# Kernel tuning notes

Measured on AMD Instinct MI355X. Metric: run time of the kernel, lower is better.

Reference implementation:

```python
import jax, jax.numpy as jnp
import numpy as np

N, L, HH, WW, E, NH = 8, 300, 96, 96, 256, 8


def setup_inputs() -> dict:
    key = jax.random.key(0)
    ks = jax.random.split(key, 9)
    return {
        "query_row": jax.random.normal(ks[0], (N, L, E), dtype=jnp.float32),
        "query_col": jax.random.normal(ks[1], (N, L, E), dtype=jnp.float32),
        "key_row": jax.random.normal(ks[2], (N, HH, WW, E), dtype=jnp.float32),
        "key_col": jax.random.normal(ks[3], (N, HH, WW, E), dtype=jnp.float32),
        "value": jax.random.normal(ks[4], (N, HH, WW, E), dtype=jnp.float32),
        "in_proj_weight": jax.random.normal(ks[5], (5 * E, E), dtype=jnp.float32) * 0.02,
        "in_proj_bias": jax.random.normal(ks[6], (5 * E,), dtype=jnp.float32) * 0.02,
        "out_proj_weight": jax.random.normal(ks[7], (E, E), dtype=jnp.float32) * 0.02,
        "out_proj_bias": jax.random.normal(ks[8], (E,), dtype=jnp.float32) * 0.02,
        "num_heads": NH,
    }


def reference(query_row, query_col, key_row, key_col, value,
              in_proj_weight, in_proj_bias, out_proj_weight, out_proj_bias,
              num_heads):
    bsz, tgt_len, embed_dim = query_row.shape
    head_dim = embed_dim // num_heads
    scaling = float(head_dim) ** -0.5

    def proj(x, i):
        w = in_proj_weight[i * embed_dim:(i + 1) * embed_dim]
        b = in_proj_bias[i * embed_dim:(i + 1) * embed_dim]
        return x @ w.T + b

    q_row = proj(query_row, 0) * scaling          # (N, L, E)
    q_col = proj(query_col, 1) * scaling          # (N, L, E)
    k_row = proj(key_row, 2).mean(axis=1)         # mean over H -> (N, W, E)
    k_col = proj(key_col, 3).mean(axis=2)         # mean over W -> (N, H, E)
    v = proj(value, 4)                            # (N, H, W, E)

    heads = lambda t: t.reshape(*t.shape[:-1], num_heads, head_dim)
    qr, qc, kr, kc = heads(q_row), heads(q_col), heads(k_row), heads(k_col)
    vh = heads(v)                                 # (N, H, W, nh, hd)

    # additive row/col decomposed scores -> independent softmaxes
    w_row = jax.nn.softmax(jnp.einsum('blnd,bwnd->bnlw', qr, kr), axis=-1)  # (N,nh,L,W)
    w_col = jax.nn.softmax(jnp.einsum('blnd,bhnd->bnlh', qc, kc), axis=-1)  # (N,nh,L,H)

    # contract col weights with value over H, then row weights over W
    tmp = jnp.einsum('bnlh,bhwnd->bnlwd', w_col, vh)       # (N,nh,L,W,hd)
    out = jnp.einsum('bnlw,bnlwd->blnd', w_row, tmp)       # (N,L,nh,hd)
    out = out.reshape(bsz, tgt_len, embed_dim).transpose(1, 0, 2)  # (L,N,E)
    return out @ out_proj_weight.T + out_proj_bias
```

## Files before the change

kernel.cpp:

```cpp
#include <hip/hip_runtime.h>
#include <cstdint>


typedef __attribute__((ext_vector_type(8))) short short8v;
typedef __attribute__((ext_vector_type(4))) short short4v;
typedef __attribute__((ext_vector_type(4))) float f32x4;

#define SCALE_Q 0.17677669529663687f

#define GLL16(gp, lp)                                                   \
  __builtin_amdgcn_global_load_lds(                                     \
      (const __attribute__((address_space(1))) void*)(gp),              \
      (__attribute__((address_space(3))) void*)(lp), 16, 0, 0)

__device__ __forceinline__ unsigned short f2bf(float x) {
  unsigned int u = __builtin_bit_cast(unsigned int, x);
  u += 0x7FFFu + ((u >> 16) & 1u);
  return (unsigned short)(u >> 16);
}

__device__ __forceinline__ unsigned int cvtpk(float a, float b) {
  unsigned int r;
  asm("v_cvt_pk_bf16_f32 %0, %1, %2" : "=v"(r) : "v"(a), "v"(b));
  return r;
}

__device__ __forceinline__ short8v pack8cvt(const f32x4& lo, const f32x4& hi) {
  union { short8v s; unsigned int u[4]; } z;
  z.u[0] = cvtpk(lo[0], lo[1]);
  z.u[1] = cvtpk(lo[2], lo[3]);
  z.u[2] = cvtpk(hi[0], hi[1]);
  z.u[3] = cvtpk(hi[2], hi[3]);
  return z.s;
}

__device__ __forceinline__ short4v pack4cvt(float a, float b, float c, float d) {
  union { short4v s; unsigned int u[2]; } z;
  z.u[0] = cvtpk(a, b);
  z.u[1] = cvtpk(c, d);
  return z.s;
}

__device__ __forceinline__ short8v pack8(const float4& fa, const float4& fb) {
  short8v v;
  v[0] = (short)f2bf(fa.x); v[1] = (short)f2bf(fa.y);
  v[2] = (short)f2bf(fa.z); v[3] = (short)f2bf(fa.w);
  v[4] = (short)f2bf(fb.x); v[5] = (short)f2bf(fb.y);
  v[6] = (short)f2bf(fb.z); v[7] = (short)f2bf(fb.w);
  return v;
}

__global__ __launch_bounds__(256) void cvt_w_kernel(const float* __restrict__ w_in,
                                                    const float* __restrict__ w_out,
                                                    short* __restrict__ Wb) {
  int idx = blockIdx.x * 256 + threadIdx.x;
  float v = (idx < 327680) ? w_in[idx] : w_out[idx - 327680];
  Wb[idx] = (short)f2bf(v);
}

__global__ __launch_bounds__(256) void mean_over_h_v3(const float* __restrict__ in,
                                                      float* __restrict__ out) {
  __shared__ float4 part[256];
  int bw = blockIdx.x;
  int b = bw / 96, w = bw - b * 96;
  int t = threadIdx.x, e4 = t & 63, hq = t >> 6;
  const float4* p = (const float4*)(in + ((size_t)b * 9216 + w) * 256) + e4 +
                    (size_t)hq * 24 * 6144;
  float4 s = {0.f, 0.f, 0.f, 0.f};
#pragma unroll
  for (int i = 0; i < 24; ++i) {
    float4 v = p[(size_t)i * 6144];
    s.x += v.x; s.y += v.y; s.z += v.z; s.w += v.w;
  }
  part[t] = s;
  __syncthreads();
  if (t < 64) {
    float4 a = part[t], c = part[t + 64], d = part[t + 128], e = part[t + 192];
    float4 o;
    o.x = (a.x + c.x + d.x + e.x) * (1.f / 96.f);
    o.y = (a.y + c.y + d.y + e.y) * (1.f / 96.f);
    o.z = (a.z + c.z + d.z + e.z) * (1.f / 96.f);
    o.w = (a.w + c.w + d.w + e.w) * (1.f / 96.f);
    ((float4*)out)[(size_t)bw * 64 + t] = o;
  }
}

__global__ __launch_bounds__(256) void mean_over_w_v3(const float* __restrict__ in,
                                                      float* __restrict__ out) {
  __shared__ float4 part[256];
  int bh = blockIdx.x;
  int t = threadIdx.x, e4 = t & 63, wq = t >> 6;
  const float4* p = (const float4*)(in + (size_t)bh * 24576) + e4 + (size_t)wq * 24 * 64;
  float4 s = {0.f, 0.f, 0.f, 0.f};
#pragma unroll
  for (int i = 0; i < 24; ++i) {
    float4 v = p[(size_t)i * 64];
    s.x += v.x; s.y += v.y; s.z += v.z; s.w += v.w;
  }
  part[t] = s;
  __syncthreads();
  if (t < 64) {
    float4 a = part[t], c = part[t + 64], d = part[t + 128], e = part[t + 192];
    float4 o;
    o.x = (a.x + c.x + d.x + e.x) * (1.f / 96.f);
    o.y = (a.y + c.y + d.y + e.y) * (1.f / 96.f);
    o.z = (a.z + c.z + d.z + e.z) * (1.f / 96.f);
    o.w = (a.w + c.w + d.w + e.w) * (1.f / 96.f);
    ((float4*)out)[(size_t)bh * 64 + t] = o;
  }
}

__global__ __launch_bounds__(256) void gemm_proj(
    const float* __restrict__ A0, const float* __restrict__ A1,
    const float* __restrict__ Aadd,
    const short* __restrict__ Wb, const float* __restrict__ bias,
    float* __restrict__ Cf, short* __restrict__ Cb0, short* __restrict__ Cb1,
    float scale, int mode) {
  __shared__ short As[32 * 264];
  int y = blockIdx.y;
  const float* A = y ? A1 : A0;
  short* Cb = y ? Cb1 : Cb0;
  const short* Wp = Wb + y * 65536;
  const float* bp = bias + y * 256;
  int t = threadIdx.x;
  int m0 = blockIdx.x * 32;
  int wave = t >> 6, lane = t & 63, r = lane & 15, g = lane >> 4;

  {
    int row = t >> 3, c0 = (t & 7) * 32;
    size_t off = ((size_t)m0 + row) * 256 + c0;
    const float* ap = A + off;
    float4 ld[8];
#pragma unroll
    for (int j = 0; j < 8; ++j) ld[j] = *(const float4*)(ap + j * 4);
    if (Aadd) {
      const float* aq = Aadd + off;
#pragma unroll
      for (int j = 0; j < 8; ++j) {
        float4 e = *(const float4*)(aq + j * 4);
        ld[j].x += e.x; ld[j].y += e.y; ld[j].z += e.z; ld[j].w += e.w;
      }
    }
    short* dst = &As[row * 264 + c0];
#pragma unroll
    for (int j = 0; j < 4; ++j)
      *(short8v*)(dst + j * 8) = pack8(ld[2 * j], ld[2 * j + 1]);
  }
  __syncthreads();

  f32x4 acc[2][4] = {};
  const short* wbase = Wp + (size_t)(wave * 64 + r) * 256;
#pragma unroll
  for (int ks = 0; ks < 8; ++ks) {
    short8v af0 = *(const short8v*)&As[r * 264 + ks * 32 + g * 8];
    short8v af1 = *(const short8v*)&As[(16 + r) * 264 + ks * 32 + g * 8];
    short8v bf[4];
#pragma unroll
    for (int nf = 0; nf < 4; ++nf)
      bf[nf] = *(const short8v*)(wbase + nf * 16 * 256 + ks * 32 + g * 8);
#pragma unroll
    for (int nf = 0; nf < 4; ++nf) {
      acc[0][nf] = __builtin_amdgcn_mfma_f32_16x16x32_bf16(af0, bf[nf], acc[0][nf], 0, 0, 0);
      acc[1][nf] = __builtin_amdgcn_mfma_f32_16x16x32_bf16(af1, bf[nf], acc[1][nf], 0, 0, 0);
    }
  }

#pragma unroll
  for (int mf = 0; mf < 2; ++mf)
#pragma unroll
    for (int nf = 0; nf < 4; ++nf) {
      int nn = wave * 64 + nf * 16 + r;
      float bval = bp[nn];
#pragma unroll
      for (int i = 0; i < 4; ++i) {
        int m = m0 + mf * 16 + g * 4 + i;
        float val = (acc[mf][nf][i] + bval) * scale;
        if (mode == 1) {
          int bb = m / 300, ll = m - bb * 300;
          Cf[((size_t)ll * 8 + bb) * 256 + nn] = val;
        } else {
          Cb[(size_t)m * 256 + nn] = (short)f2bf(val);
        }
      }
    }
}

__global__ __launch_bounds__(512, 4) void vproj_kernel(
    const float* __restrict__ A, const short* __restrict__ Wb,
    const float* __restrict__ bias, short* __restrict__ vvT) {
  __shared__ float buf[2][16 * 260];
  __shared__ short Ts[8][32 * 36];
  int t = threadIdx.x;
  int wave = t >> 6, lane = t & 63, r = lane & 15, g = lane >> 4;
  int m0g = blockIdx.x * 96;
  int b_ = blockIdx.x / 96;
  int hw00 = (blockIdx.x - b_ * 96) * 96;
  int chbase = wave * 32;

  short8v bf[8][2];
  {
    const short* wbase = Wb + (size_t)(chbase + r) * 256;
#pragma unroll
    for (int ks = 0; ks < 8; ++ks)
#pragma unroll
      for (int nf = 0; nf < 2; ++nf)
        bf[ks][nf] = *(const short8v*)(wbase + nf * 16 * 256 + ks * 32 + g * 8);
  }
#pragma unroll
  for (int ks = 0; ks < 8; ++ks)
#pragma unroll
    for (int nf = 0; nf < 2; ++nf)
      asm volatile("" : "+a"(bf[ks][nf]));
  float bias_v[2];
#pragma unroll
  for (int nf = 0; nf < 2; ++nf) bias_v[nf] = bias[chbase + nf * 16 + r];

#pragma unroll
  for (int q = 0; q < 2; ++q) {
#pragma unroll
    for (int i = 0; i < 2; ++i) {
      int row = wave * 2 + i;
      const float* gp = A + ((size_t)m0g + q * 16 + row) * 256 + lane * 4;
      GLL16(gp, &buf[q][row * 260]);
    }
  }

  int chg = chbase + (lane & 31);
  int half = lane >> 5;
  short* vbase = vvT + (size_t)(b_ * 8 + (chg >> 5)) * 294912 +
                 (size_t)(chg & 31) * 9216 + hw00;
  const short* tsr = &Ts[wave][(lane & 31) * 36];

#pragma unroll
  for (int tt = 0; tt < 6; ++tt) {
    if (tt == 5)                  asm volatile("s_waitcnt vmcnt(0)" ::: "memory");
    else if (tt == 2 || tt == 4)  asm volatile("s_waitcnt vmcnt(4)" ::: "memory");
    else                          asm volatile("s_waitcnt vmcnt(2)" ::: "memory");
    __builtin_amdgcn_s_barrier();

    f32x4 acc[2] = {};
    const float* bp_ = &buf[tt & 1][0];
#pragma unroll
    for (int ks = 0; ks < 8; ++ks) {
      const float* p = bp_ + r * 260 + ks * 32 + g * 8;
      f32x4 lo = *(const f32x4*)p;
      f32x4 hi = *(const f32x4*)(p + 4);
      short8v af = pack8cvt(lo, hi);
      acc[0] = __builtin_amdgcn_mfma_f32_16x16x32_bf16(af, bf[ks][0], acc[0], 0, 0, 0);
      acc[1] = __builtin_amdgcn_mfma_f32_16x16x32_bf16(af, bf[ks][1], acc[1], 0, 0, 0);
    }

#pragma unroll
    for (int nf = 0; nf < 2; ++nf) {
      float bv = bias_v[nf];
      *(short4v*)&Ts[wave][(nf * 16 + r) * 36 + (tt & 1) * 16 + g * 4] =
          pack4cvt(acc[nf][0] + bv, acc[nf][1] + bv, acc[nf][2] + bv, acc[nf][3] + bv);
    }
    asm volatile("" ::: "memory");

    if (tt & 1) {
      short* gdst = vbase + (tt - 1) * 16 + half * 16;
      const short* src = tsr + half * 16;
      *(short8v*)gdst = *(const short8v*)src;
      *(short8v*)(gdst + 8) = *(const short8v*)(src + 8);
      asm volatile("" ::: "memory");
    }

    __builtin_amdgcn_s_barrier();
    if (tt + 2 < 6) {
#pragma unroll
      for (int i = 0; i < 2; ++i) {
        int row = wave * 2 + i;
        const float* gp = A + ((size_t)m0g + (tt + 2) * 16 + row) * 256 + lane * 4;
        GLL16(gp, &buf[tt & 1][row * 260]);
      }
    }
  }
}

__global__ __launch_bounds__(64) void scores_softmax_v2(
    const short* __restrict__ qrb, const short* __restrict__ qcb,
    const short* __restrict__ krb, const short* __restrict__ kcb,
    short* __restrict__ wrowB, float* __restrict__ wcolT) {
  int lchunk = blockIdx.x, bn = blockIdx.y, kind = blockIdx.z;
  int b = bn >> 3, n = bn & 7;
  int lane = threadIdx.x;
  int r = lane & 15, g = lane >> 4;
  const short* qb = kind ? qcb : qrb;
  const short* kb = kind ? kcb : krb;
  int l0 = lchunk * 80;

  short8v a[5], bfr[6];
#pragma unroll
  for (int lf = 0; lf < 5; ++lf) {
    int l = l0 + lf * 16 + r;
    if (l > 299) l = 299;
    a[lf] = *(const short8v*)(qb + ((size_t)b * 300 + l) * 256 + n * 32 + g * 8);
  }
#pragma unroll
  for (int f = 0; f < 6; ++f)
    bfr[f] = *(const short8v*)(kb + ((size_t)b * 96 + f * 16 + r) * 256 + n * 32 + g * 8);

  f32x4 c[5][6];
#pragma unroll
  for (int lf = 0; lf < 5; ++lf)
#pragma unroll
    for (int f = 0; f < 6; ++f) {
      f32x4 z = {};
      c[lf][f] = __builtin_amdgcn_mfma_f32_16x16x32_bf16(a[lf], bfr[f], z, 0, 0, 0);
    }

#pragma unroll
  for (int lf = 0; lf < 5; ++lf)
#pragma unroll
    for (int i = 0; i < 4; ++i) {
      float m = c[lf][0][i];
#pragma unroll
      for (int f = 1; f < 6; ++f) m = fmaxf(m, c[lf][f][i]);
#pragma unroll
      for (int mask = 1; mask <= 8; mask <<= 1) m = fmaxf(m, __shfl_xor(m, mask, 64));
      float e[6], s = 0.f;
#pragma unroll
      for (int f = 0; f < 6; ++f) { e[f] = __expf(c[lf][f][i] - m); s += e[f]; }
#pragma unroll
      for (int mask = 1; mask <= 8; mask <<= 1) s += __shfl_xor(s, mask, 64);
      float inv = 1.f / s;
#pragma unroll
      for (int f = 0; f < 6; ++f) c[lf][f][i] = e[f] * inv;
    }

  if (kind == 0) {
#pragma unroll
    for (int lf = 0; lf < 5; ++lf)
#pragma unroll
      for (int i = 0; i < 4; ++i) {
        int l = l0 + lf * 16 + g * 4 + i;
        bool ok = (l < 300);
#pragma unroll
        for (int f = 0; f < 6; ++f) {
          float wv = ok ? c[lf][f][i] : 0.f;
          wrowB[((size_t)bn * 320 + l) * 96 + f * 16 + r] = (short)f2bf(wv);
        }
      }
  } else {
#pragma unroll
    for (int lf = 0; lf < 5; ++lf)
#pragma unroll
      for (int f = 0; f < 6; ++f) {
        int l = l0 + lf * 16 + g * 4;
        f32x4 wv = c[lf][f];
#pragma unroll
        for (int i = 0; i < 4; ++i) if (l + i >= 300) wv[i] = 0.f;
        *(f32x4*)(wcolT + ((size_t)bn * 96 + f * 16 + r) * 320 + l) = wv;
      }
  }
}

__global__ __launch_bounds__(512, 2) void attn_kernel(
    const short* __restrict__ wrowB, const float* __restrict__ wcolT,
    const short* __restrict__ vvT, float* __restrict__ part0,
    float* __restrict__ part1) {
  __shared__ f32x4 cmb[3][2][4][64];
  int i = blockIdx.x;
  int xcd = i & 7, j = i >> 3;
  int grp = j / 10, rem = j - grp * 10;
  int bn = grp * 8 + xcd;
  int lh = rem >> 1, hh2 = rem & 1;
  int b = bn >> 3, n = bn & 7;
  int t = threadIdx.x, wave = t >> 6, lane = t & 63;
  int df = wave & 1, hq = wave >> 1;
  int lbase = lh * 64;
  int r = lane & 15, g = lane >> 4;
  int hbase = hh2 * 48 + hq * 12;

  short8v a[4][3];
  const short* wr = wrowB + (size_t)bn * 320 * 96;
#pragma unroll
  for (int lf = 0; lf < 4; ++lf)
#pragma unroll
    for (int ks = 0; ks < 3; ++ks)
      a[lf][ks] = *(const short8v*)(wr + (lbase + lf * 16 + r) * 96 + ks * 32 + g * 8);

  const short* vb = vvT + (size_t)bn * 294912 + (size_t)(df * 16 + r) * 9216 + hbase * 96;
  const float* wcb = wcolT + ((size_t)bn * 96 + hbase) * 320 + lbase + g * 4;

  f32x4 acc[4] = {};
  short8v b0[3], b1[3];
  f32x4 w0[4], w1[4];
#pragma unroll
  for (int ks = 0; ks < 3; ++ks) b0[ks] = *(const short8v*)(vb + ks * 32 + g * 8);
#pragma unroll
  for (int lf = 0; lf < 4; ++lf) w0[lf] = *(const f32x4*)(wcb + lf * 16);

#pragma unroll
  for (int h2 = 0; h2 < 6; ++h2) {
    int h = h2 * 2;
#pragma unroll
    for (int ks = 0; ks < 3; ++ks) b1[ks] = *(const short8v*)(vb + (h + 1) * 96 + ks * 32 + g * 8);
#pragma unroll
    for (int lf = 0; lf < 4; ++lf) w1[lf] = *(const f32x4*)(wcb + (h + 1) * 320 + lf * 16);
    {
      f32x4 R[4] = {};
#pragma unroll
      for (int ks = 0; ks < 3; ++ks)
#pragma unroll
        for (int lf = 0; lf < 4; ++lf)
          R[lf] = __builtin_amdgcn_mfma_f32_16x16x32_bf16(a[lf][ks], b0[ks], R[lf], 0, 0, 0);
#pragma unroll
      for (int lf = 0; lf < 4; ++lf) acc[lf] += w0[lf] * R[lf];
    }
    if (h2 < 5) {
#pragma unroll
      for (int ks = 0; ks < 3; ++ks) b0[ks] = *(const short8v*)(vb + (h + 2) * 96 + ks * 32 + g * 8);
#pragma unroll
      for (int lf = 0; lf < 4; ++lf) w0[lf] = *(const f32x4*)(wcb + (h + 2) * 320 + lf * 16);
    }
    {
      f32x4 R[4] = {};
#pragma unroll
      for (int ks = 0; ks < 3; ++ks)
#pragma unroll
        for (int lf = 0; lf < 4; ++lf)
          R[lf] = __builtin_amdgcn_mfma_f32_16x16x32_bf16(a[lf][ks], b1[ks], R[lf], 0, 0, 0);
#pragma unroll
      for (int lf = 0; lf < 4; ++lf) acc[lf] += w1[lf] * R[lf];
    }
  }

  if (hq > 0) {
#pragma unroll
    for (int lf = 0; lf < 4; ++lf) cmb[hq - 1][df][lf][lane] = acc[lf];
  }
  __syncthreads();
  if (hq == 0) {
    float* po = hh2 ? part1 : part0;
#pragma unroll
    for (int lf = 0; lf < 4; ++lf) {
      f32x4 o = acc[lf];
#pragma unroll
      for (int q = 0; q < 3; ++q) o += cmb[q][df][lf][lane];
#pragma unroll
      for (int i2 = 0; i2 < 4; ++i2) {
        int l = lbase + lf * 16 + g * 4 + i2;
        if (l < 300)
          po[((size_t)b * 300 + l) * 256 + n * 32 + df * 16 + r] = o[i2];
      }
    }
  }
}

extern "C" void kernel_launch(void* const* d_in, const int* in_sizes, int n_in,
                              void* d_out, int out_size, void* d_ws, size_t ws_size,
                              hipStream_t stream) {
  const float* query_row = (const float*)d_in[0];
  const float* query_col = (const float*)d_in[1];
  const float* key_row   = (const float*)d_in[2];
  const float* key_col   = (const float*)d_in[3];
  const float* value     = (const float*)d_in[4];
  const float* W         = (const float*)d_in[5];
  const float* Bv        = (const float*)d_in[6];
  const float* Wout      = (const float*)d_in[7];
  const float* Bout      = (const float*)d_in[8];

  float* ws = (float*)d_ws;
  float* krm   = ws;
  float* kcm   = krm + 196608;
  float* part0 = kcm + 196608;
  float* part1 = part0 + 614400;
  float* wcolT = part1 + 614400;
  short* qrb   = (short*)(wcolT + 1966080);
  short* qcb   = qrb + 614400;
  short* krb   = qcb + 614400;
  short* kcb   = krb + 196608;
  short* wrowB = kcb + 196608;
  short* vvT   = wrowB + 1966080;
  short* Wb    = vvT + 18874368;

  cvt_w_kernel<<<1536, 256, 0, stream>>>(W, Wout, Wb);
  mean_over_h_v3<<<768, 256, 0, stream>>>(key_row, krm);
  mean_over_w_v3<<<768, 256, 0, stream>>>(key_col, kcm);
  gemm_proj<<<dim3(75, 2), 256, 0, stream>>>(query_row, query_col, nullptr, Wb, Bv,
                                             nullptr, qrb, qcb, SCALE_Q, 3);
  gemm_proj<<<dim3(24, 2), 256, 0, stream>>>(krm, kcm, nullptr, Wb + 131072, Bv + 512,
                                             nullptr, krb, kcb, 1.f, 3);
  vproj_kernel<<<768, 512, 0, stream>>>(value, Wb + 262144, Bv + 1024, vvT);
  scores_softmax_v2<<<dim3(4, 64, 2), 64, 0, stream>>>(qrb, qcb, krb, kcb, wrowB, wcolT);
  attn_kernel<<<640, 512, 0, stream>>>(wrowB, wcolT, vvT, part0, part1);
  gemm_proj<<<dim3(75, 1), 256, 0, stream>>>(part0, nullptr, part1, Wb + 327680, Bout,
                                             (float*)d_out, nullptr, nullptr, 1.f, 1);
}
```

Measured before the change: 157.7 us.

## Merge value projection with key means and batch the small projection GEMMs

The value projection and the two key mean reductions now run in one kernel: even blocks do the V projection and odd blocks do the row or column means, which cuts two launches and lets the memory-bound reductions overlap with the MFMA work. The four query and key projection GEMMs are merged into one 512-thread launch that dispatches on block index, and the output projection uses a 512-thread variant with bounds clamping. The goal is fewer kernel launches and less idle tail time. In exchange, the interleaved blocks use different shared-memory and register amounts, which may hurt occupancy of the heavy V path.

```diff
diff --git a/kernel.cpp b/kernel.cpp
--- a/kernel.cpp
+++ b/kernel.cpp
@@ -58,90 +58,184 @@
   Wb[idx] = (short)f2bf(v);
 }
 
-__global__ __launch_bounds__(256) void mean_over_h_v3(const float* __restrict__ in,
-                                                      float* __restrict__ out) {
-  __shared__ float4 part[256];
-  int bw = blockIdx.x;
-  int b = bw / 96, w = bw - b * 96;
-  int t = threadIdx.x, e4 = t & 63, hq = t >> 6;
-  const float4* p = (const float4*)(in + ((size_t)b * 9216 + w) * 256) + e4 +
-                    (size_t)hq * 24 * 6144;
-  float4 s = {0.f, 0.f, 0.f, 0.f};
-#pragma unroll
-  for (int i = 0; i < 24; ++i) {
-    float4 v = p[(size_t)i * 6144];
-    s.x += v.x; s.y += v.y; s.z += v.z; s.w += v.w;
-  }
-  part[t] = s;
-  __syncthreads();
-  if (t < 64) {
-    float4 a = part[t], c = part[t + 64], d = part[t + 128], e = part[t + 192];
-    float4 o;
-    o.x = (a.x + c.x + d.x + e.x) * (1.f / 96.f);
-    o.y = (a.y + c.y + d.y + e.y) * (1.f / 96.f);
-    o.z = (a.z + c.z + d.z + e.z) * (1.f / 96.f);
-    o.w = (a.w + c.w + d.w + e.w) * (1.f / 96.f);
-    ((float4*)out)[(size_t)bw * 64 + t] = o;
-  }
-}
-
-__global__ __launch_bounds__(256) void mean_over_w_v3(const float* __restrict__ in,
-                                                      float* __restrict__ out) {
-  __shared__ float4 part[256];
-  int bh = blockIdx.x;
-  int t = threadIdx.x, e4 = t & 63, wq = t >> 6;
-  const float4* p = (const float4*)(in + (size_t)bh * 24576) + e4 + (size_t)wq * 24 * 64;
-  float4 s = {0.f, 0.f, 0.f, 0.f};
-#pragma unroll
-  for (int i = 0; i < 24; ++i) {
-    float4 v = p[(size_t)i * 64];
-    s.x += v.x; s.y += v.y; s.z += v.z; s.w += v.w;
-  }
-  part[t] = s;
-  __syncthreads();
-  if (t < 64) {
-    float4 a = part[t], c = part[t + 64], d = part[t + 128], e = part[t + 192];
-    float4 o;
-    o.x = (a.x + c.x + d.x + e.x) * (1.f / 96.f);
-    o.y = (a.y + c.y + d.y + e.y) * (1.f / 96.f);
-    o.z = (a.z + c.z + d.z + e.z) * (1.f / 96.f);
-    o.w = (a.w + c.w + d.w + e.w) * (1.f / 96.f);
-    ((float4*)out)[(size_t)bh * 64 + t] = o;
-  }
-}
-
-__global__ __launch_bounds__(256) void gemm_proj(
-    const float* __restrict__ A0, const float* __restrict__ A1,
-    const float* __restrict__ Aadd,
-    const short* __restrict__ Wb, const float* __restrict__ bias,
-    float* __restrict__ Cf, short* __restrict__ Cb0, short* __restrict__ Cb1,
-    float scale, int mode) {
-  __shared__ short As[32 * 264];
-  int y = blockIdx.y;
-  const float* A = y ? A1 : A0;
-  short* Cb = y ? Cb1 : Cb0;
-  const short* Wp = Wb + y * 65536;
-  const float* bp = bias + y * 256;
+__global__ __launch_bounds__(512, 4) void mega1_kernel(
+    const float* __restrict__ A, const short* __restrict__ Wb,
+    const float* __restrict__ bias, short* __restrict__ vvT,
+    const float* __restrict__ key_row, const float* __restrict__ key_col,
+    float* __restrict__ krm, float* __restrict__ kcm) {
+  __shared__ float buf[2][16 * 260];
+  __shared__ short Ts[8][32 * 36];
+  int blk = blockIdx.x;
   int t = threadIdx.x;
-  int m0 = blockIdx.x * 32;
-  int wave = t >> 6, lane = t & 63, r = lane & 15, g = lane >> 4;
+
+  if ((blk & 1) == 0) {
+    int vb_id = blk >> 1;
+    int wave = t >> 6, lane = t & 63, r = lane & 15, g = lane >> 4;
+    int m0g = vb_id * 96;
+    int b_ = vb_id / 96;
+    int hw00 = (vb_id - b_ * 96) * 96;
+    int chbase = wave * 32;
+
+    short8v bf[8][2];
+    {
+      const short* wbase = Wb + (size_t)(chbase + r) * 256;
+#pragma unroll
+      for (int ks = 0; ks < 8; ++ks)
+#pragma unroll
+        for (int nf = 0; nf < 2; ++nf)
+          bf[ks][nf] = *(const short8v*)(wbase + nf * 16 * 256 + ks * 32 + g * 8);
+    }
+#pragma unroll
+    for (int ks = 0; ks < 8; ++ks)
+#pragma unroll
+      for (int nf = 0; nf < 2; ++nf)
+        asm volatile("" : "+a"(bf[ks][nf]));
+    float bias_v[2];
+#pragma unroll
+    for (int nf = 0; nf < 2; ++nf) bias_v[nf] = bias[chbase + nf * 16 + r];
+
+#pragma unroll
+    for (int q = 0; q < 2; ++q) {
+#pragma unroll
+      for (int i = 0; i < 2; ++i) {
+        int row = wave * 2 + i;
+        const float* gp = A + ((size_t)m0g + q * 16 + row) * 256 + lane * 4;
+        GLL16(gp, &buf[q][row * 260]);
+      }
+    }
+
+    int chg = chbase + (lane & 31);
+    int half = lane >> 5;
+    short* vbase = vvT + (size_t)(b_ * 8 + (chg >> 5)) * 294912 +
+                   (size_t)(chg & 31) * 9216 + hw00;
+    const short* tsr = &Ts[wave][(lane & 31) * 36];
+
+#pragma unroll
+    for (int tt = 0; tt < 6; ++tt) {
+      if (tt == 5)                  asm volatile("s_waitcnt vmcnt(0)" ::: "memory");
+      else if (tt == 2 || tt == 4)  asm volatile("s_waitcnt vmcnt(4)" ::: "memory");
+      else                          asm volatile("s_waitcnt vmcnt(2)" ::: "memory");
+      __builtin_amdgcn_s_barrier();
+
+      f32x4 acc[2] = {};
+      const float* bp_ = &buf[tt & 1][0];
+#pragma unroll
+      for (int ks = 0; ks < 8; ++ks) {
+        const float* p = bp_ + r * 260 + ks * 32 + g * 8;
+        f32x4 lo = *(const f32x4*)p;
+        f32x4 hi = *(const f32x4*)(p + 4);
+        short8v af = pack8cvt(lo, hi);
+        acc[0] = __builtin_amdgcn_mfma_f32_16x16x32_bf16(af, bf[ks][0], acc[0], 0, 0, 0);
+        acc[1] = __builtin_amdgcn_mfma_f32_16x16x32_bf16(af, bf[ks][1], acc[1], 0, 0, 0);
+      }
+
+#pragma unroll
+      for (int nf = 0; nf < 2; ++nf) {
+        float bv = bias_v[nf];
+        *(short4v*)&Ts[wave][(nf * 16 + r) * 36 + (tt & 1) * 16 + g * 4] =
+            pack4cvt(acc[nf][0] + bv, acc[nf][1] + bv, acc[nf][2] + bv, acc[nf][3] + bv);
+      }
+      asm volatile("" ::: "memory");
+
+      if (tt & 1) {
+        short* gdst = vbase + (tt - 1) * 16 + half * 16;
+        const short* src = tsr + half * 16;
+        *(short8v*)gdst = *(const short8v*)src;
+        *(short8v*)(gdst + 8) = *(const short8v*)(src + 8);
+        asm volatile("" ::: "memory");
+      }
+
+      __builtin_amdgcn_s_barrier();
+      if (tt + 2 < 6) {
+#pragma unroll
+        for (int i = 0; i < 2; ++i) {
+          int row = wave * 2 + i;
+          const float* gp = A + ((size_t)m0g + (tt + 2) * 16 + row) * 256 + lane * 4;
+          GLL16(gp, &buf[tt & 1][row * 260]);
+        }
+      }
+    }
+  } else {
+    int id = blk >> 1;
+    int sub = t >> 8, u = t & 255;
+    int e4 = u & 63, q4 = u >> 6;
+    float4* part4 = (float4*)&buf[0][0];
+    if (id < 384) {
+      int bw = id * 2 + sub;
+      int b = bw / 96, w = bw - b * 96;
+      const float4* p = (const float4*)(key_row + ((size_t)b * 9216 + w) * 256) +
+                        e4 + (size_t)q4 * 24 * 6144;
+      float4 s = {0.f, 0.f, 0.f, 0.f};
+#pragma unroll
+      for (int i = 0; i < 24; ++i) {
+        float4 v = p[(size_t)i * 6144];
+        s.x += v.x; s.y += v.y; s.z += v.z; s.w += v.w;
+      }
+      part4[sub * 256 + u] = s;
+      __syncthreads();
+      if (u < 64) {
+        float4 a = part4[sub * 256 + u], c = part4[sub * 256 + u + 64];
+        float4 d = part4[sub * 256 + u + 128], e = part4[sub * 256 + u + 192];
+        float4 o;
+        o.x = (a.x + c.x + d.x + e.x) * (1.f / 96.f);
+        o.y = (a.y + c.y + d.y + e.y) * (1.f / 96.f);
+        o.z = (a.z + c.z + d.z + e.z) * (1.f / 96.f);
+        o.w = (a.w + c.w + d.w + e.w) * (1.f / 96.f);
+        ((float4*)krm)[(size_t)bw * 64 + u] = o;
+      }
+    } else {
+      int bh = (id - 384) * 2 + sub;
+      const float4* p = (const float4*)(key_col + (size_t)bh * 24576) + e4 +
+                        (size_t)q4 * 24 * 64;
+      float4 s = {0.f, 0.f, 0.f, 0.f};
+#pragma unroll
+      for (int i = 0; i < 24; ++i) {
+        float4 v = p[(size_t)i * 64];
+        s.x += v.x; s.y += v.y; s.z += v.z; s.w += v.w;
+      }
+      part4[sub * 256 + u] = s;
+      __syncthreads();
+      if (u < 64) {
+        float4 a = part4[sub * 256 + u], c = part4[sub * 256 + u + 64];
+        float4 d = part4[sub * 256 + u + 128], e = part4[sub * 256 + u + 192];
+        float4 o;
+        o.x = (a.x + c.x + d.x + e.x) * (1.f / 96.f);
+        o.y = (a.y + c.y + d.y + e.y) * (1.f / 96.f);
+        o.z = (a.z + c.z + d.z + e.z) * (1.f / 96.f);
+        o.w = (a.w + c.w + d.w + e.w) * (1.f / 96.f);
+        ((float4*)kcm)[(size_t)bh * 64 + u] = o;
+      }
+    }
+  }
+}
+
+__global__ __launch_bounds__(512) void gemm512(
+    const float* __restrict__ krm, const float* __restrict__ kcm,
+    const float* __restrict__ qrow, const float* __restrict__ qcol,
+    const short* __restrict__ Wb, const float* __restrict__ Bv,
+    short* __restrict__ krb, short* __restrict__ kcb,
+    short* __restrict__ qrb, short* __restrict__ qcb) {
+  __shared__ short As[2][32 * 264];
+  int id = blockIdx.x;
+  const float* A; short* Cb; const short* Wp; const float* bp; int M, m064;
+  float scale;
+  if (id < 12)      { A = krm;  Cb = krb; Wp = Wb + 131072; bp = Bv + 512; M = 768;  m064 = id * 64;        scale = 1.f; }
+  else if (id < 24) { A = kcm;  Cb = kcb; Wp = Wb + 196608; bp = Bv + 768; M = 768;  m064 = (id - 12) * 64; scale = 1.f; }
+  else if (id < 62) { A = qrow; Cb = qrb; Wp = Wb;          bp = Bv;       M = 2400; m064 = (id - 24) * 64; scale = SCALE_Q; }
+  else              { A = qcol; Cb = qcb; Wp = Wb + 65536;  bp = Bv + 256; M = 2400; m064 = (id - 62) * 64; scale = SCALE_Q; }
+
+  int t = threadIdx.x, sub = t >> 8, u = t & 255;
+  int wave = u >> 6, lane = u & 63, r = lane & 15, g = lane >> 4;
+  int m0 = m064 + sub * 32;
 
   {
-    int row = t >> 3, c0 = (t & 7) * 32;
-    size_t off = ((size_t)m0 + row) * 256 + c0;
-    const float* ap = A + off;
+    int row = u >> 3, c0 = (u & 7) * 32;
+    int mrow = m0 + row; if (mrow >= M) mrow = M - 1;
+    const float* ap = A + (size_t)mrow * 256 + c0;
     float4 ld[8];
 #pragma unroll
     for (int j = 0; j < 8; ++j) ld[j] = *(const float4*)(ap + j * 4);
-    if (Aadd) {
-      const float* aq = Aadd + off;
-#pragma unroll
-      for (int j = 0; j < 8; ++j) {
-        float4 e = *(const float4*)(aq + j * 4);
-        ld[j].x += e.x; ld[j].y += e.y; ld[j].z += e.z; ld[j].w += e.w;
-      }
-    }
-    short* dst = &As[row * 264 + c0];
+    short* dst = &As[sub][row * 264 + c0];
 #pragma unroll
     for (int j = 0; j < 4; ++j)
       *(short8v*)(dst + j * 8) = pack8(ld[2 * j], ld[2 * j + 1]);
@@ -152,8 +246,8 @@
   const short* wbase = Wp + (size_t)(wave * 64 + r) * 256;
 #pragma unroll
   for (int ks = 0; ks < 8; ++ks) {
-    short8v af0 = *(const short8v*)&As[r * 264 + ks * 32 + g * 8];
-    short8v af1 = *(const short8v*)&As[(16 + r) * 264 + ks * 32 + g * 8];
+    short8v af0 = *(const short8v*)&As[sub][r * 264 + ks * 32 + g * 8];
+    short8v af1 = *(const short8v*)&As[sub][(16 + r) * 264 + ks * 32 + g * 8];
     short8v bf[4];
 #pragma unroll
     for (int nf = 0; nf < 4; ++nf)
@@ -174,108 +268,74 @@
 #pragma unroll
       for (int i = 0; i < 4; ++i) {
         int m = m0 + mf * 16 + g * 4 + i;
-        float val = (acc[mf][nf][i] + bval) * scale;
-        if (mode == 1) {
-          int bb = m / 300, ll = m - bb * 300;
-          Cf[((size_t)ll * 8 + bb) * 256 + nn] = val;
-        } else {
-          Cb[(size_t)m * 256 + nn] = (short)f2bf(val);
-        }
-      }
-    }
-}
-
-__global__ __launch_bounds__(512, 4) void vproj_kernel(
-    const float* __restrict__ A, const short* __restrict__ Wb,
-    const float* __restrict__ bias, short* __restrict__ vvT) {
-  __shared__ float buf[2][16 * 260];
-  __shared__ short Ts[8][32 * 36];
-  int t = threadIdx.x;
-  int wave = t >> 6, lane = t & 63, r = lane & 15, g = lane >> 4;
-  int m0g = blockIdx.x * 96;
-  int b_ = blockIdx.x / 96;
-  int hw00 = (blockIdx.x - b_ * 96) * 96;
-  int chbase = wave * 32;
-
-  short8v bf[8][2];
+        if (m >= M) continue;
+        Cb[(size_t)m * 256 + nn] = (short)f2bf((acc[mf][nf][i] + bval) * scale);
+      }
+    }
+}
+
+__global__ __launch_bounds__(512) void gemm512_out(
+    const float* __restrict__ A0, const float* __restrict__ Aadd,
+    const short* __restrict__ Wp, const float* __restrict__ bp,
+    float* __restrict__ Cf) {
+  __shared__ short As[2][32 * 264];
+  const int M = 2400;
+  int t = threadIdx.x, sub = t >> 8, u = t & 255;
+  int wave = u >> 6, lane = u & 63, r = lane & 15, g = lane >> 4;
+  int m0 = blockIdx.x * 64 + sub * 32;
+
   {
-    const short* wbase = Wb + (size_t)(chbase + r) * 256;
-#pragma unroll
-    for (int ks = 0; ks < 8; ++ks)
-#pragma unroll
-      for (int nf = 0; nf < 2; ++nf)
-        bf[ks][nf] = *(const short8v*)(wbase + nf * 16 * 256 + ks * 32 + g * 8);
-  }
-#pragma unroll
-  for (int ks = 0; ks < 8; ++ks)
-#pragma unroll
-    for (int nf = 0; nf < 2; ++nf)
-      asm volatile("" : "+a"(bf[ks][nf]));
-  float bias_v[2];
-#pragma unroll
-  for (int nf = 0; nf < 2; ++nf) bias_v[nf] = bias[chbase + nf * 16 + r];
-
-#pragma unroll
-  for (int q = 0; q < 2; ++q) {
-#pragma unroll
-    for (int i = 0; i < 2; ++i) {
-      int row = wave * 2 + i;
-      const float* gp = A + ((size_t)m0g + q * 16 + row) * 256 + lane * 4;
-      GLL16(gp, &buf[q][row * 260]);
-    }
-  }
-
-  int chg = chbase + (lane & 31);
-  int half = lane >> 5;
-  short* vbase = vvT + (size_t)(b_ * 8 + (chg >> 5)) * 294912 +
-                 (size_t)(chg & 31) * 9216 + hw00;
-  const short* tsr = &Ts[wave][(lane & 31) * 36];
-
-#pragma unroll
-  for (int tt = 0; tt < 6; ++tt) {
-    if (tt == 5)                  asm volatile("s_waitcnt vmcnt(0)" ::: "memory");
-    else if (tt == 2 || tt == 4)  asm volatile("s_waitcnt vmcnt(4)" ::: "memory");
-    else                          asm volatile("s_waitcnt vmcnt(2)" ::: "memory");
-    __builtin_amdgcn_s_barrier();
-
-    f32x4 acc[2] = {};
-    const float* bp_ = &buf[tt & 1][0];
-#pragma unroll
-    for (int ks = 0; ks < 8; ++ks) {
-      const float* p = bp_ + r * 260 + ks * 32 + g * 8;
-      f32x4 lo = *(const f32x4*)p;
-      f32x4 hi = *(const f32x4*)(p + 4);
-      short8v af = pack8cvt(lo, hi);
-      acc[0] = __builtin_amdgcn_mfma_f32_16x16x32_bf16(af, bf[ks][0], acc[0], 0, 0, 0);
-      acc[1] = __builtin_amdgcn_mfma_f32_16x16x32_bf16(af, bf[ks][1], acc[1], 0, 0, 0);
-    }
-
-#pragma unroll
-    for (int nf = 0; nf < 2; ++nf) {
-      float bv = bias_v[nf];
-      *(short4v*)&Ts[wave][(nf * 16 + r) * 36 + (tt & 1) * 16 + g * 4] =
-          pack4cvt(acc[nf][0] + bv, acc[nf][1] + bv, acc[nf][2] + bv, acc[nf][3] + bv);
-    }
-    asm volatile("" ::: "memory");
-
-    if (tt & 1) {
-      short* gdst = vbase + (tt - 1) * 16 + half * 16;
-      const short* src = tsr + half * 16;
-      *(short8v*)gdst = *(const short8v*)src;
-      *(short8v*)(gdst + 8) = *(const short8v*)(src + 8);
-      asm volatile("" ::: "memory");
-    }
-
-    __builtin_amdgcn_s_barrier();
-    if (tt + 2 < 6) {
-#pragma unroll
-      for (int i = 0; i < 2; ++i) {
-        int row = wave * 2 + i;
-        const float* gp = A + ((size_t)m0g + (tt + 2) * 16 + row) * 256 + lane * 4;
-        GLL16(gp, &buf[tt & 1][row * 260]);
-      }
-    }
-  }
+    int row = u >> 3, c0 = (u & 7) * 32;
+    int mrow = m0 + row; if (mrow >= M) mrow = M - 1;
+    size_t off = (size_t)mrow * 256 + c0;
+    const float* ap = A0 + off;
+    const float* aq = Aadd + off;
+    float4 ld[8];
+#pragma unroll
+    for (int j = 0; j < 8; ++j) {
+      float4 x = *(const float4*)(ap + j * 4);
+      float4 e = *(const float4*)(aq + j * 4);
+      x.x += e.x; x.y += e.y; x.z += e.z; x.w += e.w;
+      ld[j] = x;
+    }
+    short* dst = &As[sub][row * 264 + c0];
+#pragma unroll
+    for (int j = 0; j < 4; ++j)
+      *(short8v*)(dst + j * 8) = pack8(ld[2 * j], ld[2 * j + 1]);
+  }
+  __syncthreads();
+
+  f32x4 acc[2][4] = {};
+  const short* wbase = Wp + (size_t)(wave * 64 + r) * 256;
+#pragma unroll
+  for (int ks = 0; ks < 8; ++ks) {
+    short8v af0 = *(const short8v*)&As[sub][r * 264 + ks * 32 + g * 8];
+    short8v af1 = *(const short8v*)&As[sub][(16 + r) * 264 + ks * 32 + g * 8];
+    short8v bf[4];
+#pragma unroll
+    for (int nf = 0; nf < 4; ++nf)
+      bf[nf] = *(const short8v*)(wbase + nf * 16 * 256 + ks * 32 + g * 8);
+#pragma unroll
+    for (int nf = 0; nf < 4; ++nf) {
+      acc[0][nf] = __builtin_amdgcn_mfma_f32_16x16x32_bf16(af0, bf[nf], acc[0][nf], 0, 0, 0);
+      acc[1][nf] = __builtin_amdgcn_mfma_f32_16x16x32_bf16(af1, bf[nf], acc[1][nf], 0, 0, 0);
+    }
+  }
+
+#pragma unroll
+  for (int mf = 0; mf < 2; ++mf)
+#pragma unroll
+    for (int nf = 0; nf < 4; ++nf) {
+      int nn = wave * 64 + nf * 16 + r;
+      float bval = bp[nn];
+#pragma unroll
+      for (int i = 0; i < 4; ++i) {
+        int m = m0 + mf * 16 + g * 4 + i;
+        if (m >= M) continue;
+        int bb = m / 300, ll = m - bb * 300;
+        Cf[((size_t)ll * 8 + bb) * 256 + nn] = acc[mf][nf][i] + bval;
+      }
+    }
 }
 
 __global__ __launch_bounds__(64) void scores_softmax_v2(
@@ -477,15 +537,11 @@
   short* Wb    = vvT + 18874368;
 
   cvt_w_kernel<<<1536, 256, 0, stream>>>(W, Wout, Wb);
-  mean_over_h_v3<<<768, 256, 0, stream>>>(key_row, krm);
-  mean_over_w_v3<<<768, 256, 0, stream>>>(key_col, kcm);
-  gemm_proj<<<dim3(75, 2), 256, 0, stream>>>(query_row, query_col, nullptr, Wb, Bv,
-                                             nullptr, qrb, qcb, SCALE_Q, 3);
-  gemm_proj<<<dim3(24, 2), 256, 0, stream>>>(krm, kcm, nullptr, Wb + 131072, Bv + 512,
-                                             nullptr, krb, kcb, 1.f, 3);
-  vproj_kernel<<<768, 512, 0, stream>>>(value, Wb + 262144, Bv + 1024, vvT);
+  mega1_kernel<<<1536, 512, 0, stream>>>(value, Wb + 262144, Bv + 1024, vvT,
+                                         key_row, key_col, krm, kcm);
+  gemm512<<<100, 512, 0, stream>>>(krm, kcm, query_row, query_col, Wb, Bv,
+                                   krb, kcb, qrb, qcb);
   scores_softmax_v2<<<dim3(4, 64, 2), 64, 0, stream>>>(qrb, qcb, krb, kcb, wrowB, wcolT);
   attn_kernel<<<640, 512, 0, stream>>>(wrowB, wcolT, vvT, part0, part1);
-  gemm_proj<<<dim3(75, 1), 256, 0, stream>>>(part0, nullptr, part1, Wb + 327680, Bout,
-                                             (float*)d_out, nullptr, nullptr, 1.f, 1);
-}
+  gemm512_out<<<38, 512, 0, stream>>>(part0, part1, Wb + 327680, Bout, (float*)d_out);
+}
```

Result: no change. 155.4 us (-1.5%).
